# Kernel tuning notes

Hardware: AMD Instinct MI355X
Metric: run time of the kernel (lower is better)

The kernel has to match this reference:

```python
import jax, jax.numpy as jnp
import numpy as np

B = 2
Z, Y, X = 21, 256, 256          # spatial_shape (z, y, x)
OZ, OY, OX = 10, 128, 128       # strided conv output grid: floor((in+2p-3)/2)+1
CIN, C1, C2 = 16, 32, 64
N = 400_000
EPS = 1e-3                      # BN eps from norm_cfg


def setup_inputs() -> dict:
    rng = np.random.default_rng(0)
    total = B * Z * Y * X
    lin = rng.choice(total, size=N, replace=False)
    lin.sort()
    b = (lin // (Z * Y * X)).astype(np.int64)
    r = lin % (Z * Y * X)
    z = r // (Y * X)
    r = r % (Y * X)
    y = r // X
    x = r % X
    coors = np.stack([b, z, y, x], axis=1).astype(np.int32)

    # Active output coords of SparseConv3d(k=3, s=2, pad=[0,1,1]):
    # input c is seen by output o iff o*2 - p + j == c for some j in {0,1,2}.
    pads = (0, 1, 1)
    cand_dims = []
    for c, p, osz in zip((z, y, x), pads, (OZ, OY, OX)):
        per = []
        for j in range(3):
            num = c + p - j
            o = num // 2
            valid = (num % 2 == 0) & (num >= 0) & (o < osz)
            per.append((o, valid))
        cand_dims.append(per)
    cand = []
    for oz, vz in cand_dims[0]:
        for oy, vy in cand_dims[1]:
            for ox, vx in cand_dims[2]:
                v = vz & vy & vx
                if v.any():
                    cand.append(np.stack([b[v], oz[v], oy[v], ox[v]], axis=1))
    out_coors = np.unique(np.concatenate(cand, axis=0), axis=0).astype(np.int32)

    key = jax.random.key(0)
    ks = jax.random.split(key, 11)
    voxel_feat = jax.random.normal(ks[0], (N, CIN), jnp.float32)
    W1 = jax.random.normal(ks[1], (27, CIN, C1), jnp.float32) / np.float32(np.sqrt(27 * CIN))
    W2 = jax.random.normal(ks[2], (27, C1, C2), jnp.float32) / np.float32(np.sqrt(27 * C1))
    g1 = 1.0 + 0.1 * jax.random.normal(ks[3], (C1,), jnp.float32)
    b1 = 0.1 * jax.random.normal(ks[4], (C1,), jnp.float32)
    m1 = 0.1 * jax.random.normal(ks[5], (C1,), jnp.float32)
    v1 = 0.5 + jnp.abs(jax.random.normal(ks[6], (C1,), jnp.float32)) * 0.5
    g2 = 1.0 + 0.1 * jax.random.normal(ks[7], (C2,), jnp.float32)
    b2 = 0.1 * jax.random.normal(ks[8], (C2,), jnp.float32)
    m2 = 0.1 * jax.random.normal(ks[9], (C2,), jnp.float32)
    v2 = 0.5 + jnp.abs(jax.random.normal(ks[10], (C2,), jnp.float32)) * 0.5
    return {
        "voxel_feat": voxel_feat,
        "coors": jnp.asarray(coors),
        "out_coors": jnp.asarray(out_coors),
        "W1": W1, "g1": g1, "b1": b1, "m1": m1, "v1": v1,
        "W2": W2, "g2": g2, "b2": b2, "m2": m2, "v2": v2,
        "batch_size": B,
    }


def _bn_relu(x, g, b, m, v):
    return jax.nn.relu((x - m) * (g * jax.lax.rsqrt(v + EPS)) + b)


def _build_grid(coors, n):
    # dense hash of active voxels -> row index (rulebook lookup table)
    lin = ((coors[:, 0] * Z + coors[:, 1]) * Y + coors[:, 2]) * X + coors[:, 3]
    return jnp.full((B * Z * Y * X,), -1, jnp.int32).at[lin].set(jnp.arange(n, dtype=jnp.int32))


def _sparse_conv(feat, grid, bcol, zz, yy, xx, W, cout):
    # gather-GEMM-scatter for one kernel offset set; loop over 27 offsets is structural
    n = zz[0].shape[0]
    out = jnp.zeros((n, cout), feat.dtype)
    for k in range(27):
        z_, y_, x_ = zz[k], yy[k], xx[k]
        ok = (z_ >= 0) & (z_ < Z) & (y_ >= 0) & (y_ < Y) & (x_ >= 0) & (x_ < X)
        l = ((bcol * Z + jnp.clip(z_, 0, Z - 1)) * Y + jnp.clip(y_, 0, Y - 1)) * X + jnp.clip(x_, 0, X - 1)
        idx = grid[l]
        ok = ok & (idx >= 0)
        f = feat[jnp.where(ok, idx, 0)]
        out = out + jnp.where(ok[:, None], f @ W[k], jnp.zeros((), feat.dtype))
    return out


def reference(voxel_feat, coors, out_coors, W1, g1, b1, m1, v1, W2, g2, b2, m2, v2, batch_size):
    n = voxel_feat.shape[0]
    grid = _build_grid(coors, n)

    # --- SubMConv3d(k=3, pad=1): out[c] = sum_j W1[j] @ in[c + j - 1], outputs only at input sites
    zz, yy, xx = [], [], []
    for dz in (-1, 0, 1):
        for dy in (-1, 0, 1):
            for dx in (-1, 0, 1):
                zz.append(coors[:, 1] + dz)
                yy.append(coors[:, 2] + dy)
                xx.append(coors[:, 3] + dx)
    f1 = _bn_relu(_sparse_conv(voxel_feat, grid, coors[:, 0], zz, yy, xx, W1, C1), g1, b1, m1, v1)

    # --- SparseConv3d(k=3, s=2, pad=[0,1,1]): input coord = o*2 - p + j
    zz, yy, xx = [], [], []
    for jz in range(3):
        for jy in range(3):
            for jx in range(3):
                zz.append(out_coors[:, 1] * 2 - 0 + jz)
                yy.append(out_coors[:, 2] * 2 - 1 + jy)
                xx.append(out_coors[:, 3] * 2 - 1 + jx)
    f2 = _bn_relu(_sparse_conv(f1, grid, out_coors[:, 0], zz, yy, xx, W2, C2), g2, b2, m2, v2)

    return f2, out_coors, batch_size
```

## Files before the change

### kernel.cpp

```cpp
#include <hip/hip_runtime.h>

#define ZD 21
#define YD 256
#define XD 256
#define BD 2
#define NCIN 16
#define NC1 32
#define NC2 64
#define BN_EPS 1e-3f

#define ZP 23
#define YP 258
#define XP 258
#define YPXP 66564
#define GRID_TOT (BD * ZP * YPXP)
#define TAILN 133647

typedef __attribute__((ext_vector_type(8))) short short8;
typedef __attribute__((ext_vector_type(4))) float floatx4;

__constant__ int KOFF[36] = {
    0, 1, 2, 258, 259, 260, 516, 517, 518,
    66564, 66565, 66566, 66822, 66823, 66824, 67080, 67081, 67082,
    133128, 133129, 133130, 133386, 133387, 133388, 133644, 133645, 133646,
    0, 0, 0, 0, 0, 0, 0, 0, 0};

__device__ inline unsigned short rne_bf16(float w) {
    unsigned b = __float_as_uint(w);
    return (unsigned short)((b + 0x7FFFu + ((b >> 16) & 1u)) >> 16);
}

__device__ inline void lds_barrier() {
    asm volatile("s_waitcnt lgkmcnt(0)" ::: "memory");
    __builtin_amdgcn_s_barrier();
}

__device__ inline int xcd_swz(int b, int nwg) {
    const int q = nwg >> 3, r = nwg & 7;
    const int xcd = b & 7, slot = b >> 3;
    return (xcd < r ? xcd * (q + 1) : r * (q + 1) + (xcd - r) * q) + slot;
}

__global__ __launch_bounds__(256) void prep_k(
    const float* __restrict__ feat, const int* __restrict__ coors,
    const float* __restrict__ W1, const float* __restrict__ W2,
    const int* __restrict__ oc, const int* __restrict__ bs,
    int* __restrict__ grid, unsigned short* __restrict__ featb,
    unsigned short* __restrict__ f1,
    short* __restrict__ wp1, short* __restrict__ wp2,
    float* __restrict__ out2, int n, int m4) {
    const int i = blockIdx.x * 256 + threadIdx.x;

    if (i < n) {
        const int4 c = ((const int4*)coors)[i];
        grid[((c.x * ZP + c.y + 1) * YP + c.z + 1) * XP + c.w + 1] = i + 1;
    }
    if (i < 2 * n) {
        const float4* p = (const float4*)feat + (size_t)i * 2;
        const float4 a = p[0], b = p[1];
        short8 o;
        o[0] = (short)rne_bf16(a.x); o[1] = (short)rne_bf16(a.y);
        o[2] = (short)rne_bf16(a.z); o[3] = (short)rne_bf16(a.w);
        o[4] = (short)rne_bf16(b.x); o[5] = (short)rne_bf16(b.y);
        o[6] = (short)rne_bf16(b.z); o[7] = (short)rne_bf16(b.w);
        ((short8*)featb)[i + 2] = o;
    }
    if (i < 2) ((short8*)featb)[i] = (short8)0;
    if (i < 4) ((short8*)f1)[i] = (short8)0;
    if (i < 14 * 2 * 512) {
        int pair = i / 1024, r = i % 1024, cb = r / 512, e = r % 512;
        int lane = e / 8, j = e % 8, kk = (lane >> 4) * 8 + j;
        int ko = pair * 2 + (kk >> 4), ci = kk & 15, co = cb * 16 + (lane & 15);
        float w = (ko < 27) ? W1[(ko * NCIN + ci) * NC1 + co] : 0.f;
        wp1[(pair * 2 + cb) * 512 + e] = (short)rne_bf16(w);
    }
    const int t2 = i - 14 * 2 * 512;
    if (t2 >= 0 && t2 < 27 * 4 * 512) {
        int k = t2 / 2048, r = t2 % 2048, cb = r / 512, e = r % 512;
        int lane = e / 8, j = e % 8, ci = (lane >> 4) * 8 + j, co = cb * 16 + (lane & 15);
        wp2[(k * 4 + cb) * 512 + e] = (short)rne_bf16(W2[(k * NC1 + ci) * NC2 + co]);
    }
    if (i < m4) out2[i] = (float)oc[i];
    if (i == m4) out2[m4] = (float)bs[0];
}

__global__ __launch_bounds__(256, 4) void conv1_k(
    const unsigned short* __restrict__ featb, const int* __restrict__ coors,
    const short* __restrict__ wp1,
    const float* __restrict__ g1, const float* __restrict__ b1,
    const float* __restrict__ m1, const float* __restrict__ v1,
    const int* __restrict__ gridp, unsigned short* __restrict__ f1, int n, int tail0) {
    const int tid = threadIdx.x;
    const int lane = tid & 63;
    const int quad = lane >> 4;
    const int mrow = lane & 15;
    const int bid = xcd_swz(blockIdx.x, gridDim.x);
    const int vbase = bid * 128 + (tid >> 6) * 32;
    const int ko_add = quad >> 1;
    const int ci_half = quad & 1;

    __shared__ short lw[2][2048];

    int pb[2];
#pragma unroll
    for (int mt = 0; mt < 2; ++mt) {
        const int v = vbase + mt * 16 + mrow;
        if (v < n) {
            const int4 cc = ((const int4*)coors)[v];
            pb[mt] = ((cc.x * ZP + cc.y) * YP + cc.z) * XP + cc.w;
        } else {
            pb[mt] = tail0;
        }
    }

    floatx4 d[2][2];
#pragma unroll
    for (int mt = 0; mt < 2; ++mt)
#pragma unroll
        for (int cb = 0; cb < 2; ++cb) d[mt][cb] = (floatx4){0.f, 0.f, 0.f, 0.f};

    const short8* __restrict__ wg = (const short8*)wp1;

    ((short8*)lw[0])[tid] = wg[tid];
    int id_c[2], id_n[2];
#pragma unroll
    for (int mt = 0; mt < 2; ++mt) id_c[mt] = gridp[pb[mt] + KOFF[ko_add]];
#pragma unroll
    for (int mt = 0; mt < 2; ++mt) id_n[mt] = gridp[pb[mt] + KOFF[2 + ko_add]];
    short8 a_c[2];
#pragma unroll
    for (int mt = 0; mt < 2; ++mt)
        a_c[mt] = *(const short8*)(featb + (unsigned)(id_c[mt] * NCIN + ci_half * 8));
    lds_barrier();

    int buf = 0;
#pragma unroll 1
    for (int s = 0; s < 7; ++s) {
        short8 wreg;
#pragma unroll
        for (int p = 0; p < 2; ++p) {
            const int pr = 2 * s + p;
            if (p == 0 && s < 6) wreg = wg[(s + 1) * 256 + tid];

            const short8 wf0 = ((const short8*)lw[buf])[p * 128 + lane];
            const short8 wf1 = ((const short8*)lw[buf])[p * 128 + 64 + lane];

            short8 a_nx[2];
#pragma unroll
            for (int mt = 0; mt < 2; ++mt)
                a_nx[mt] = *(const short8*)(featb + (unsigned)(id_n[mt] * NCIN + ci_half * 8));

            int id_f[2];
            {
                const int koff = KOFF[2 * (pr + 2) + ko_add];
#pragma unroll
                for (int mt = 0; mt < 2; ++mt) id_f[mt] = gridp[pb[mt] + koff];
            }

#pragma unroll
            for (int mt = 0; mt < 2; ++mt) {
                d[mt][0] = __builtin_amdgcn_mfma_f32_16x16x32_bf16(a_c[mt], wf0, d[mt][0], 0, 0, 0);
                d[mt][1] = __builtin_amdgcn_mfma_f32_16x16x32_bf16(a_c[mt], wf1, d[mt][1], 0, 0, 0);
            }
#pragma unroll
            for (int mt = 0; mt < 2; ++mt) { a_c[mt] = a_nx[mt]; id_n[mt] = id_f[mt]; }
        }
        if (s < 6) ((short8*)lw[buf ^ 1])[tid] = wreg;
        lds_barrier();
        buf ^= 1;
    }

    const int col = lane & 15;
#pragma unroll
    for (int cb = 0; cb < 2; ++cb) {
        const int ch = cb * 16 + col;
        const float sc = g1[ch] * rsqrtf(v1[ch] + BN_EPS);
        const float sb = b1[ch] - m1[ch] * sc;
#pragma unroll
        for (int mt = 0; mt < 2; ++mt) {
#pragma unroll
            for (int r = 0; r < 4; ++r) {
                const int v = vbase + mt * 16 + quad * 4 + r;
                if (v < n) {
                    const float o = fmaxf(fmaf(d[mt][cb][r], sc, sb), 0.f);
                    f1[(unsigned)((v + 1) * NC1 + ch)] = rne_bf16(o);
                }
            }
        }
    }
}

__global__ __launch_bounds__(256, 4) void conv2_k(
    const unsigned short* __restrict__ f1,
    const int* __restrict__ ocoors, const short* __restrict__ wp2,
    const float* __restrict__ g2, const float* __restrict__ b2,
    const float* __restrict__ m2, const float* __restrict__ v2,
    const int* __restrict__ gridp, float* __restrict__ out, int m, int tail0) {
    const int tid = threadIdx.x;
    const int lane = tid & 63;
    const int quad = lane >> 4;
    const int mrow = lane & 15;
    const int bid = xcd_swz(blockIdx.x, gridDim.x);
    const int vbase = bid * 128 + (tid >> 6) * 32;

    __shared__ short lw[2][6144];

    int pb[2];
#pragma unroll
    for (int mt = 0; mt < 2; ++mt) {
        const int v = vbase + mt * 16 + mrow;
        if (v < m) {
            const int4 cc = ((const int4*)ocoors)[v];
            pb[mt] = ((cc.x * ZP + 2 * cc.y + 1) * YP + 2 * cc.z) * XP + 2 * cc.w;
        } else {
            pb[mt] = tail0;
        }
    }

    floatx4 d[2][4];
#pragma unroll
    for (int mt = 0; mt < 2; ++mt)
#pragma unroll
        for (int cb = 0; cb < 4; ++cb) d[mt][cb] = (floatx4){0.f, 0.f, 0.f, 0.f};

    const short8* __restrict__ wg = (const short8*)wp2;

    ((short8*)lw[0])[tid] = wg[tid];
    ((short8*)lw[0])[256 + tid] = wg[256 + tid];
    ((short8*)lw[0])[512 + tid] = wg[512 + tid];
    int id_c[2], id_n[2];
#pragma unroll
    for (int mt = 0; mt < 2; ++mt) id_c[mt] = gridp[pb[mt] + KOFF[0]];
#pragma unroll
    for (int mt = 0; mt < 2; ++mt) id_n[mt] = gridp[pb[mt] + KOFF[1]];
    short8 a_c[2];
#pragma unroll
    for (int mt = 0; mt < 2; ++mt)
        a_c[mt] = *(const short8*)(f1 + (unsigned)(id_c[mt] * NC1 + quad * 8));
    lds_barrier();

    int buf = 0;
#pragma unroll 1
    for (int s = 0; s < 9; ++s) {
        short8 wreg[3];
#pragma unroll
        for (int t = 0; t < 3; ++t) {
            const int tap = 3 * s + t;
            if (s < 8) wreg[t] = wg[((s + 1) * 3 + t) * 256 + tid];

            short8 wf[4];
#pragma unroll
            for (int cb = 0; cb < 4; ++cb)
                wf[cb] = ((const short8*)lw[buf])[t * 256 + cb * 64 + lane];

            short8 a_nx[2];
#pragma unroll
            for (int mt = 0; mt < 2; ++mt)
                a_nx[mt] = *(const short8*)(f1 + (unsigned)(id_n[mt] * NC1 + quad * 8));

            int id_f[2];
            {
                const int koff = KOFF[tap + 2];
#pragma unroll
                for (int mt = 0; mt < 2; ++mt) id_f[mt] = gridp[pb[mt] + koff];
            }

#pragma unroll
            for (int mt = 0; mt < 2; ++mt) {
#pragma unroll
                for (int cb = 0; cb < 4; ++cb)
                    d[mt][cb] = __builtin_amdgcn_mfma_f32_16x16x32_bf16(a_c[mt], wf[cb], d[mt][cb], 0, 0, 0);
            }
#pragma unroll
            for (int mt = 0; mt < 2; ++mt) { a_c[mt] = a_nx[mt]; id_n[mt] = id_f[mt]; }
        }
        if (s < 8) {
#pragma unroll
            for (int t = 0; t < 3; ++t)
                ((short8*)lw[buf ^ 1])[t * 256 + tid] = wreg[t];
        }
        lds_barrier();
        buf ^= 1;
    }

    const int col = lane & 15;
#pragma unroll
    for (int cb = 0; cb < 4; ++cb) {
        const int ch = cb * 16 + col;
        const float sc = g2[ch] * rsqrtf(v2[ch] + BN_EPS);
        const float sb = b2[ch] - m2[ch] * sc;
#pragma unroll
        for (int mt = 0; mt < 2; ++mt) {
#pragma unroll
            for (int r = 0; r < 4; ++r) {
                const int v = vbase + mt * 16 + quad * 4 + r;
                if (v < m)
                    out[(unsigned)(v * NC2 + ch)] = fmaxf(fmaf(d[mt][cb][r], sc, sb), 0.f);
            }
        }
    }
}

extern "C" void kernel_launch(void* const* d_in, const int* in_sizes, int n_in,
                              void* d_out, int out_size, void* d_ws, size_t ws_size,
                              hipStream_t stream) {
    const float* feat  = (const float*)d_in[0];
    const int*   coors = (const int*)d_in[1];
    const int*   ocoors= (const int*)d_in[2];
    const float* W1 = (const float*)d_in[3];
    const float* g1 = (const float*)d_in[4];
    const float* b1 = (const float*)d_in[5];
    const float* m1 = (const float*)d_in[6];
    const float* v1 = (const float*)d_in[7];
    const float* W2 = (const float*)d_in[8];
    const float* g2 = (const float*)d_in[9];
    const float* b2 = (const float*)d_in[10];
    const float* m2 = (const float*)d_in[11];
    const float* v2 = (const float*)d_in[12];
    const int*   bs = (const int*)d_in[13];

    const int n = in_sizes[0] / NCIN;
    const int m = in_sizes[2] / 4;

    char* ws = (char*)d_ws;
    int* grid = (int*)ws;
    size_t off = ((size_t)(GRID_TOT + TAILN) * sizeof(int) + 255) & ~(size_t)255;
    unsigned short* featb = (unsigned short*)(ws + off);
    off += ((size_t)(n + 1) * NCIN * 2 + 255) & ~(size_t)255;
    unsigned short* f1 = (unsigned short*)(ws + off);
    off += ((size_t)(n + 1) * NC1 * 2 + 255) & ~(size_t)255;
    short* wp1 = (short*)(ws + off);
    off += (14 * 2 * 512 * 2 + 255) & ~(size_t)255;
    short* wp2 = (short*)(ws + off);

    float* out = (float*)d_out;
    float* out2 = out + (size_t)m * NC2;

    int prep_threads = 2 * n;
    if (m * 4 + 1 > prep_threads) prep_threads = m * 4 + 1;

    hipMemsetAsync(grid, 0x00, (size_t)(GRID_TOT + TAILN) * sizeof(int), stream);
    prep_k<<<(prep_threads + 255) / 256, 256, 0, stream>>>(feat, coors, W1, W2, ocoors, bs,
                                                           grid, featb, f1, wp1, wp2, out2, n, m * 4);

    conv1_k<<<(n + 127) / 128, 256, 0, stream>>>(featb, coors, wp1, g1, b1, m1, v1,
                                                 grid, f1, n, GRID_TOT);

    conv2_k<<<(m + 127) / 128, 256, 0, stream>>>(f1, ocoors, wp2,
                                                 g2, b2, m2, v2, grid, out, m, GRID_TOT);
}
```

Baseline: 238.1 us.

## Deepen gather prefetch to a full stage ahead in both sparse convs

Restructures the software pipeline in both conv kernels so grid-index lookups run two stages ahead and feature gathers one full stage (2 or 3 taps) ahead, instead of one tap ahead. This hides more global-memory latency of the indirect gathers behind MFMA work. It needs more live registers, so conv2's launch bounds drop from 4 to 3 blocks per SM, which lowers occupancy. The KOFF table is trimmed because out-of-range padding entries are no longer read.

```diff
diff --git a/kernel.cpp b/kernel.cpp
--- a/kernel.cpp
+++ b/kernel.cpp
@@ -19,11 +19,11 @@
 typedef __attribute__((ext_vector_type(8))) short short8;
 typedef __attribute__((ext_vector_type(4))) float floatx4;
 
-__constant__ int KOFF[36] = {
+__constant__ int KOFF[28] = {
     0, 1, 2, 258, 259, 260, 516, 517, 518,
     66564, 66565, 66566, 66822, 66823, 66824, 67080, 67081, 67082,
     133128, 133129, 133130, 133386, 133387, 133388, 133644, 133645, 133646,
-    0, 0, 0, 0, 0, 0, 0, 0, 0};
+    0};
 
 __device__ inline unsigned short rne_bf16(float w) {
     unsigned b = __float_as_uint(w);
@@ -122,51 +122,64 @@
     const short8* __restrict__ wg = (const short8*)wp1;
 
     ((short8*)lw[0])[tid] = wg[tid];
-    int id_c[2], id_n[2];
-#pragma unroll
-    for (int mt = 0; mt < 2; ++mt) id_c[mt] = gridp[pb[mt] + KOFF[ko_add]];
-#pragma unroll
-    for (int mt = 0; mt < 2; ++mt) id_n[mt] = gridp[pb[mt] + KOFF[2 + ko_add]];
-    short8 a_c[2];
-#pragma unroll
-    for (int mt = 0; mt < 2; ++mt)
-        a_c[mt] = *(const short8*)(featb + (unsigned)(id_c[mt] * NCIN + ci_half * 8));
+
+    int idc[2][2], idn[2][2];
+#pragma unroll
+    for (int p = 0; p < 2; ++p)
+#pragma unroll
+        for (int mt = 0; mt < 2; ++mt)
+            idc[p][mt] = gridp[pb[mt] + KOFF[2 * p + ko_add]];
+#pragma unroll
+    for (int p = 0; p < 2; ++p)
+#pragma unroll
+        for (int mt = 0; mt < 2; ++mt)
+            idn[p][mt] = gridp[pb[mt] + KOFF[2 * (2 + p) + ko_add]];
+
+    short8 a[2][2];
+#pragma unroll
+    for (int p = 0; p < 2; ++p)
+#pragma unroll
+        for (int mt = 0; mt < 2; ++mt)
+            a[p][mt] = *(const short8*)(featb + (unsigned)(idc[p][mt] * NCIN + ci_half * 8));
     lds_barrier();
 
     int buf = 0;
 #pragma unroll 1
     for (int s = 0; s < 7; ++s) {
+        int idf[2][2];
+        if (s < 5) {
+#pragma unroll
+            for (int p = 0; p < 2; ++p)
+#pragma unroll
+                for (int mt = 0; mt < 2; ++mt)
+                    idf[p][mt] = gridp[pb[mt] + KOFF[4 * s + 8 + 2 * p + ko_add]];
+        }
         short8 wreg;
+        if (s < 6) wreg = wg[(s + 1) * 256 + tid];
+
 #pragma unroll
         for (int p = 0; p < 2; ++p) {
-            const int pr = 2 * s + p;
-            if (p == 0 && s < 6) wreg = wg[(s + 1) * 256 + tid];
-
             const short8 wf0 = ((const short8*)lw[buf])[p * 128 + lane];
             const short8 wf1 = ((const short8*)lw[buf])[p * 128 + 64 + lane];
-
-            short8 a_nx[2];
-#pragma unroll
-            for (int mt = 0; mt < 2; ++mt)
-                a_nx[mt] = *(const short8*)(featb + (unsigned)(id_n[mt] * NCIN + ci_half * 8));
-
-            int id_f[2];
-            {
-                const int koff = KOFF[2 * (pr + 2) + ko_add];
-#pragma unroll
-                for (int mt = 0; mt < 2; ++mt) id_f[mt] = gridp[pb[mt] + koff];
-            }
-
 #pragma unroll
             for (int mt = 0; mt < 2; ++mt) {
-                d[mt][0] = __builtin_amdgcn_mfma_f32_16x16x32_bf16(a_c[mt], wf0, d[mt][0], 0, 0, 0);
-                d[mt][1] = __builtin_amdgcn_mfma_f32_16x16x32_bf16(a_c[mt], wf1, d[mt][1], 0, 0, 0);
-            }
-#pragma unroll
-            for (int mt = 0; mt < 2; ++mt) { a_c[mt] = a_nx[mt]; id_n[mt] = id_f[mt]; }
+                d[mt][0] = __builtin_amdgcn_mfma_f32_16x16x32_bf16(a[p][mt], wf0, d[mt][0], 0, 0, 0);
+                d[mt][1] = __builtin_amdgcn_mfma_f32_16x16x32_bf16(a[p][mt], wf1, d[mt][1], 0, 0, 0);
+            }
+            if (s < 6) {
+#pragma unroll
+                for (int mt = 0; mt < 2; ++mt)
+                    a[p][mt] = *(const short8*)(featb + (unsigned)(idn[p][mt] * NCIN + ci_half * 8));
+            }
         }
         if (s < 6) ((short8*)lw[buf ^ 1])[tid] = wreg;
         lds_barrier();
+        if (s < 5) {
+#pragma unroll
+            for (int p = 0; p < 2; ++p)
+#pragma unroll
+                for (int mt = 0; mt < 2; ++mt) idn[p][mt] = idf[p][mt];
+        }
         buf ^= 1;
     }
 
@@ -190,7 +203,7 @@
     }
 }
 
-__global__ __launch_bounds__(256, 4) void conv2_k(
+__global__ __launch_bounds__(256, 3) void conv2_k(
     const unsigned short* __restrict__ f1,
     const int* __restrict__ ocoors, const short* __restrict__ wp2,
     const float* __restrict__ g2, const float* __restrict__ b2,
@@ -228,51 +241,59 @@
     ((short8*)lw[0])[tid] = wg[tid];
     ((short8*)lw[0])[256 + tid] = wg[256 + tid];
     ((short8*)lw[0])[512 + tid] = wg[512 + tid];
-    int id_c[2], id_n[2];
-#pragma unroll
-    for (int mt = 0; mt < 2; ++mt) id_c[mt] = gridp[pb[mt] + KOFF[0]];
-#pragma unroll
-    for (int mt = 0; mt < 2; ++mt) id_n[mt] = gridp[pb[mt] + KOFF[1]];
-    short8 a_c[2];
-#pragma unroll
-    for (int mt = 0; mt < 2; ++mt)
-        a_c[mt] = *(const short8*)(f1 + (unsigned)(id_c[mt] * NC1 + quad * 8));
+
+    int idc[3][2], idn[3][2];
+#pragma unroll
+    for (int t = 0; t < 3; ++t)
+#pragma unroll
+        for (int mt = 0; mt < 2; ++mt) idc[t][mt] = gridp[pb[mt] + KOFF[t]];
+#pragma unroll
+    for (int t = 0; t < 3; ++t)
+#pragma unroll
+        for (int mt = 0; mt < 2; ++mt) idn[t][mt] = gridp[pb[mt] + KOFF[3 + t]];
+
+    short8 a[3][2];
+#pragma unroll
+    for (int t = 0; t < 3; ++t)
+#pragma unroll
+        for (int mt = 0; mt < 2; ++mt)
+            a[t][mt] = *(const short8*)(f1 + (unsigned)(idc[t][mt] * NC1 + quad * 8));
     lds_barrier();
 
     int buf = 0;
 #pragma unroll 1
     for (int s = 0; s < 9; ++s) {
+        int idf[3][2];
+        if (s < 7) {
+#pragma unroll
+            for (int t = 0; t < 3; ++t)
+#pragma unroll
+                for (int mt = 0; mt < 2; ++mt)
+                    idf[t][mt] = gridp[pb[mt] + KOFF[3 * s + 6 + t]];
+        }
         short8 wreg[3];
+        if (s < 8) {
+#pragma unroll
+            for (int t = 0; t < 3; ++t) wreg[t] = wg[((s + 1) * 3 + t) * 256 + tid];
+        }
+
 #pragma unroll
         for (int t = 0; t < 3; ++t) {
-            const int tap = 3 * s + t;
-            if (s < 8) wreg[t] = wg[((s + 1) * 3 + t) * 256 + tid];
-
             short8 wf[4];
 #pragma unroll
             for (int cb = 0; cb < 4; ++cb)
                 wf[cb] = ((const short8*)lw[buf])[t * 256 + cb * 64 + lane];
-
-            short8 a_nx[2];
-#pragma unroll
-            for (int mt = 0; mt < 2; ++mt)
-                a_nx[mt] = *(const short8*)(f1 + (unsigned)(id_n[mt] * NC1 + quad * 8));
-
-            int id_f[2];
-            {
-                const int koff = KOFF[tap + 2];
-#pragma unroll
-                for (int mt = 0; mt < 2; ++mt) id_f[mt] = gridp[pb[mt] + koff];
-            }
-
 #pragma unroll
             for (int mt = 0; mt < 2; ++mt) {
 #pragma unroll
                 for (int cb = 0; cb < 4; ++cb)
-                    d[mt][cb] = __builtin_amdgcn_mfma_f32_16x16x32_bf16(a_c[mt], wf[cb], d[mt][cb], 0, 0, 0);
-            }
-#pragma unroll
-            for (int mt = 0; mt < 2; ++mt) { a_c[mt] = a_nx[mt]; id_n[mt] = id_f[mt]; }
+                    d[mt][cb] = __builtin_amdgcn_mfma_f32_16x16x32_bf16(a[t][mt], wf[cb], d[mt][cb], 0, 0, 0);
+            }
+            if (s < 8) {
+#pragma unroll
+                for (int mt = 0; mt < 2; ++mt)
+                    a[t][mt] = *(const short8*)(f1 + (unsigned)(idn[t][mt] * NC1 + quad * 8));
+            }
         }
         if (s < 8) {
 #pragma unroll
@@ -280,6 +301,12 @@
                 ((short8*)lw[buf ^ 1])[t * 256 + tid] = wreg[t];
         }
         lds_barrier();
+        if (s < 7) {
+#pragma unroll
+            for (int t = 0; t < 3; ++t)
+#pragma unroll
+                for (int mt = 0; mt < 2; ++mt) idn[t][mt] = idf[t][mt];
+        }
         buf ^= 1;
     }
 
```

Result: faster. 232.9 us (-2.2%).

## Halve rows per wave and prefetch a full stage of gathers ahead

Applied to the files above, without the earlier changes.

Each wave now handles one 16-row M tile instead of two, so blocks cover 64 voxels and the grid doubles. Occupancy hints rise from 4 to 6 blocks per CU. The gather pipeline is restructured so each stage's grid-index lookups and feature loads are issued one whole stage ahead, rather than one tap ahead. The aim is to hide gather latency through more waves in flight and a deeper prefetch, at the cost of reloading the weight tile into LDS twice as often per voxel.

```diff
diff --git a/kernel.cpp b/kernel.cpp
--- a/kernel.cpp
+++ b/kernel.cpp
@@ -19,11 +19,11 @@
 typedef __attribute__((ext_vector_type(8))) short short8;
 typedef __attribute__((ext_vector_type(4))) float floatx4;
 
-__constant__ int KOFF[36] = {
+__constant__ int KOFF[28] = {
     0, 1, 2, 258, 259, 260, 516, 517, 518,
     66564, 66565, 66566, 66822, 66823, 66824, 67080, 67081, 67082,
     133128, 133129, 133130, 133386, 133387, 133388, 133644, 133645, 133646,
-    0, 0, 0, 0, 0, 0, 0, 0, 0};
+    0};
 
 __device__ inline unsigned short rne_bf16(float w) {
     unsigned b = __float_as_uint(w);
@@ -84,7 +84,7 @@
     if (i == m4) out2[m4] = (float)bs[0];
 }
 
-__global__ __launch_bounds__(256, 4) void conv1_k(
+__global__ __launch_bounds__(256, 6) void conv1_k(
     const unsigned short* __restrict__ featb, const int* __restrict__ coors,
     const short* __restrict__ wp1,
     const float* __restrict__ g1, const float* __restrict__ b1,
@@ -95,78 +95,70 @@
     const int quad = lane >> 4;
     const int mrow = lane & 15;
     const int bid = xcd_swz(blockIdx.x, gridDim.x);
-    const int vbase = bid * 128 + (tid >> 6) * 32;
+    const int vbase = bid * 64 + (tid >> 6) * 16;
     const int ko_add = quad >> 1;
     const int ci_half = quad & 1;
 
     __shared__ short lw[2][2048];
 
-    int pb[2];
-#pragma unroll
-    for (int mt = 0; mt < 2; ++mt) {
-        const int v = vbase + mt * 16 + mrow;
+    int pb;
+    {
+        const int v = vbase + mrow;
         if (v < n) {
             const int4 cc = ((const int4*)coors)[v];
-            pb[mt] = ((cc.x * ZP + cc.y) * YP + cc.z) * XP + cc.w;
+            pb = ((cc.x * ZP + cc.y) * YP + cc.z) * XP + cc.w;
         } else {
-            pb[mt] = tail0;
-        }
-    }
-
-    floatx4 d[2][2];
-#pragma unroll
-    for (int mt = 0; mt < 2; ++mt)
-#pragma unroll
-        for (int cb = 0; cb < 2; ++cb) d[mt][cb] = (floatx4){0.f, 0.f, 0.f, 0.f};
+            pb = tail0;
+        }
+    }
+
+    floatx4 d[2];
+#pragma unroll
+    for (int cb = 0; cb < 2; ++cb) d[cb] = (floatx4){0.f, 0.f, 0.f, 0.f};
 
     const short8* __restrict__ wg = (const short8*)wp1;
 
     ((short8*)lw[0])[tid] = wg[tid];
-    int id_c[2], id_n[2];
-#pragma unroll
-    for (int mt = 0; mt < 2; ++mt) id_c[mt] = gridp[pb[mt] + KOFF[ko_add]];
-#pragma unroll
-    for (int mt = 0; mt < 2; ++mt) id_n[mt] = gridp[pb[mt] + KOFF[2 + ko_add]];
-    short8 a_c[2];
-#pragma unroll
-    for (int mt = 0; mt < 2; ++mt)
-        a_c[mt] = *(const short8*)(featb + (unsigned)(id_c[mt] * NCIN + ci_half * 8));
+
+    int idc[2], idn[2];
+#pragma unroll
+    for (int p = 0; p < 2; ++p) idc[p] = gridp[pb + KOFF[2 * p + ko_add]];
+#pragma unroll
+    for (int p = 0; p < 2; ++p) idn[p] = gridp[pb + KOFF[2 * (2 + p) + ko_add]];
+
+    short8 a[2];
+#pragma unroll
+    for (int p = 0; p < 2; ++p)
+        a[p] = *(const short8*)(featb + (unsigned)(idc[p] * NCIN + ci_half * 8));
     lds_barrier();
 
     int buf = 0;
 #pragma unroll 1
     for (int s = 0; s < 7; ++s) {
+        int idf[2];
+        if (s < 5) {
+#pragma unroll
+            for (int p = 0; p < 2; ++p)
+                idf[p] = gridp[pb + KOFF[4 * s + 8 + 2 * p + ko_add]];
+        }
         short8 wreg;
+        if (s < 6) wreg = wg[(s + 1) * 256 + tid];
+
 #pragma unroll
         for (int p = 0; p < 2; ++p) {
-            const int pr = 2 * s + p;
-            if (p == 0 && s < 6) wreg = wg[(s + 1) * 256 + tid];
-
             const short8 wf0 = ((const short8*)lw[buf])[p * 128 + lane];
             const short8 wf1 = ((const short8*)lw[buf])[p * 128 + 64 + lane];
-
-            short8 a_nx[2];
-#pragma unroll
-            for (int mt = 0; mt < 2; ++mt)
-                a_nx[mt] = *(const short8*)(featb + (unsigned)(id_n[mt] * NCIN + ci_half * 8));
-
-            int id_f[2];
-            {
-                const int koff = KOFF[2 * (pr + 2) + ko_add];
-#pragma unroll
-                for (int mt = 0; mt < 2; ++mt) id_f[mt] = gridp[pb[mt] + koff];
-            }
-
-#pragma unroll
-            for (int mt = 0; mt < 2; ++mt) {
-                d[mt][0] = __builtin_amdgcn_mfma_f32_16x16x32_bf16(a_c[mt], wf0, d[mt][0], 0, 0, 0);
-                d[mt][1] = __builtin_amdgcn_mfma_f32_16x16x32_bf16(a_c[mt], wf1, d[mt][1], 0, 0, 0);
-            }
-#pragma unroll
-            for (int mt = 0; mt < 2; ++mt) { a_c[mt] = a_nx[mt]; id_n[mt] = id_f[mt]; }
+            d[0] = __builtin_amdgcn_mfma_f32_16x16x32_bf16(a[p], wf0, d[0], 0, 0, 0);
+            d[1] = __builtin_amdgcn_mfma_f32_16x16x32_bf16(a[p], wf1, d[1], 0, 0, 0);
+            if (s < 6)
+                a[p] = *(const short8*)(featb + (unsigned)(idn[p] * NCIN + ci_half * 8));
         }
         if (s < 6) ((short8*)lw[buf ^ 1])[tid] = wreg;
         lds_barrier();
+        if (s < 5) {
+#pragma unroll
+            for (int p = 0; p < 2; ++p) idn[p] = idf[p];
+        }
         buf ^= 1;
     }
 
@@ -177,20 +169,17 @@
         const float sc = g1[ch] * rsqrtf(v1[ch] + BN_EPS);
         const float sb = b1[ch] - m1[ch] * sc;
 #pragma unroll
-        for (int mt = 0; mt < 2; ++mt) {
-#pragma unroll
-            for (int r = 0; r < 4; ++r) {
-                const int v = vbase + mt * 16 + quad * 4 + r;
-                if (v < n) {
-                    const float o = fmaxf(fmaf(d[mt][cb][r], sc, sb), 0.f);
-                    f1[(unsigned)((v + 1) * NC1 + ch)] = rne_bf16(o);
-                }
+        for (int r = 0; r < 4; ++r) {
+            const int v = vbase + quad * 4 + r;
+            if (v < n) {
+                const float o = fmaxf(fmaf(d[cb][r], sc, sb), 0.f);
+                f1[(unsigned)((v + 1) * NC1 + ch)] = rne_bf16(o);
             }
         }
     }
 }
 
-__global__ __launch_bounds__(256, 4) void conv2_k(
+__global__ __launch_bounds__(256, 6) void conv2_k(
     const unsigned short* __restrict__ f1,
     const int* __restrict__ ocoors, const short* __restrict__ wp2,
     const float* __restrict__ g2, const float* __restrict__ b2,
@@ -201,78 +190,68 @@
     const int quad = lane >> 4;
     const int mrow = lane & 15;
     const int bid = xcd_swz(blockIdx.x, gridDim.x);
-    const int vbase = bid * 128 + (tid >> 6) * 32;
+    const int vbase = bid * 64 + (tid >> 6) * 16;
 
     __shared__ short lw[2][6144];
 
-    int pb[2];
-#pragma unroll
-    for (int mt = 0; mt < 2; ++mt) {
-        const int v = vbase + mt * 16 + mrow;
+    int pb;
+    {
+        const int v = vbase + mrow;
         if (v < m) {
             const int4 cc = ((const int4*)ocoors)[v];
-            pb[mt] = ((cc.x * ZP + 2 * cc.y + 1) * YP + 2 * cc.z) * XP + 2 * cc.w;
+            pb = ((cc.x * ZP + 2 * cc.y + 1) * YP + 2 * cc.z) * XP + 2 * cc.w;
         } else {
-            pb[mt] = tail0;
-        }
-    }
-
-    floatx4 d[2][4];
-#pragma unroll
-    for (int mt = 0; mt < 2; ++mt)
-#pragma unroll
-        for (int cb = 0; cb < 4; ++cb) d[mt][cb] = (floatx4){0.f, 0.f, 0.f, 0.f};
+            pb = tail0;
+        }
+    }
+
+    floatx4 d[4];
+#pragma unroll
+    for (int cb = 0; cb < 4; ++cb) d[cb] = (floatx4){0.f, 0.f, 0.f, 0.f};
 
     const short8* __restrict__ wg = (const short8*)wp2;
 
     ((short8*)lw[0])[tid] = wg[tid];
     ((short8*)lw[0])[256 + tid] = wg[256 + tid];
     ((short8*)lw[0])[512 + tid] = wg[512 + tid];
-    int id_c[2], id_n[2];
-#pragma unroll
-    for (int mt = 0; mt < 2; ++mt) id_c[mt] = gridp[pb[mt] + KOFF[0]];
-#pragma unroll
-    for (int mt = 0; mt < 2; ++mt) id_n[mt] = gridp[pb[mt] + KOFF[1]];
-    short8 a_c[2];
-#pragma unroll
-    for (int mt = 0; mt < 2; ++mt)
-        a_c[mt] = *(const short8*)(f1 + (unsigned)(id_c[mt] * NC1 + quad * 8));
+
+    int idc[3], idn[3];
+#pragma unroll
+    for (int t = 0; t < 3; ++t) idc[t] = gridp[pb + KOFF[t]];
+#pragma unroll
+    for (int t = 0; t < 3; ++t) idn[t] = gridp[pb + KOFF[3 + t]];
+
+    short8 a[3];
+#pragma unroll
+    for (int t = 0; t < 3; ++t)
+        a[t] = *(const short8*)(f1 + (unsigned)(idc[t] * NC1 + quad * 8));
     lds_barrier();
 
     int buf = 0;
 #pragma unroll 1
     for (int s = 0; s < 9; ++s) {
+        int idf[3];
+        if (s < 7) {
+#pragma unroll
+            for (int t = 0; t < 3; ++t) idf[t] = gridp[pb + KOFF[3 * s + 6 + t]];
+        }
         short8 wreg[3];
+        if (s < 8) {
+#pragma unroll
+            for (int t = 0; t < 3; ++t) wreg[t] = wg[((s + 1) * 3 + t) * 256 + tid];
+        }
+
 #pragma unroll
         for (int t = 0; t < 3; ++t) {
-            const int tap = 3 * s + t;
-            if (s < 8) wreg[t] = wg[((s + 1) * 3 + t) * 256 + tid];
-
             short8 wf[4];
 #pragma unroll
             for (int cb = 0; cb < 4; ++cb)
                 wf[cb] = ((const short8*)lw[buf])[t * 256 + cb * 64 + lane];
-
-            short8 a_nx[2];
-#pragma unroll
-            for (int mt = 0; mt < 2; ++mt)
-                a_nx[mt] = *(const short8*)(f1 + (unsigned)(id_n[mt] * NC1 + quad * 8));
-
-            int id_f[2];
-            {
-                const int koff = KOFF[tap + 2];
-#pragma unroll
-                for (int mt = 0; mt < 2; ++mt) id_f[mt] = gridp[pb[mt] + koff];
-            }
-
-#pragma unroll
-            for (int mt = 0; mt < 2; ++mt) {
-#pragma unroll
-                for (int cb = 0; cb < 4; ++cb)
-                    d[mt][cb] = __builtin_amdgcn_mfma_f32_16x16x32_bf16(a_c[mt], wf[cb], d[mt][cb], 0, 0, 0);
-            }
-#pragma unroll
-            for (int mt = 0; mt < 2; ++mt) { a_c[mt] = a_nx[mt]; id_n[mt] = id_f[mt]; }
+#pragma unroll
+            for (int cb = 0; cb < 4; ++cb)
+                d[cb] = __builtin_amdgcn_mfma_f32_16x16x32_bf16(a[t], wf[cb], d[cb], 0, 0, 0);
+            if (s < 8)
+                a[t] = *(const short8*)(f1 + (unsigned)(idn[t] * NC1 + quad * 8));
         }
         if (s < 8) {
 #pragma unroll
@@ -280,6 +259,10 @@
                 ((short8*)lw[buf ^ 1])[t * 256 + tid] = wreg[t];
         }
         lds_barrier();
+        if (s < 7) {
+#pragma unroll
+            for (int t = 0; t < 3; ++t) idn[t] = idf[t];
+        }
         buf ^= 1;
     }
 
@@ -290,13 +273,10 @@
         const float sc = g2[ch] * rsqrtf(v2[ch] + BN_EPS);
         const float sb = b2[ch] - m2[ch] * sc;
 #pragma unroll
-        for (int mt = 0; mt < 2; ++mt) {
-#pragma unroll
-            for (int r = 0; r < 4; ++r) {
-                const int v = vbase + mt * 16 + quad * 4 + r;
-                if (v < m)
-                    out[(unsigned)(v * NC2 + ch)] = fmaxf(fmaf(d[mt][cb][r], sc, sb), 0.f);
-            }
+        for (int r = 0; r < 4; ++r) {
+            const int v = vbase + quad * 4 + r;
+            if (v < m)
+                out[(unsigned)(v * NC2 + ch)] = fmaxf(fmaf(d[cb][r], sc, sb), 0.f);
         }
     }
 }
@@ -343,9 +323,9 @@
     prep_k<<<(prep_threads + 255) / 256, 256, 0, stream>>>(feat, coors, W1, W2, ocoors, bs,
                                                            grid, featb, f1, wp1, wp2, out2, n, m * 4);
 
-    conv1_k<<<(n + 127) / 128, 256, 0, stream>>>(featb, coors, wp1, g1, b1, m1, v1,
-                                                 grid, f1, n, GRID_TOT);
-
-    conv2_k<<<(m + 127) / 128, 256, 0, stream>>>(f1, ocoors, wp2,
-                                                 g2, b2, m2, v2, grid, out, m, GRID_TOT);
-}
+    conv1_k<<<(n + 63) / 64, 256, 0, stream>>>(featb, coors, wp1, g1, b1, m1, v1,
+                                               grid, f1, n, GRID_TOT);
+
+    conv2_k<<<(m + 63) / 64, 256, 0, stream>>>(f1, ocoors, wp2,
+                                               g2, b2, m2, v2, grid, out, m, GRID_TOT);
+}
```

After: 248.9 us. 4.5% more time.
